# Performance work log

Hardware: AMD Instinct MI355X
Metric: run time of the kernel (lower is better)

The kernel has to match this reference:

```python
import jax, jax.numpy as jnp
import numpy as np
from jax import lax

B, C, H, W, HEADS = 2, 256, 192, 256, 8
HS = C // 2  # hidden_size per axial branch


def setup_inputs() -> dict:
    key = jax.random.key(0)
    ks = jax.random.split(key, 12)
    f = lambda k, shape, s=0.02: jax.random.normal(k, shape, jnp.float32) * s
    return {
        "x": jax.random.normal(ks[0], (B, C, H, W), jnp.float32),
        "ln1_g": jnp.ones((C,), jnp.float32),
        "ln1_b": jnp.zeros((C,), jnp.float32),
        "conv_in_w": f(ks[1], (C, C)),
        "conv_in_b": jnp.zeros((C,), jnp.float32),
        "qkv_h_w": f(ks[2], (3 * HS, HS)),
        "qkv_h_b": jnp.zeros((3 * HS,), jnp.float32),
        "qkv_v_w": f(ks[3], (3 * HS, HS)),
        "qkv_v_b": jnp.zeros((3 * HS,), jnp.float32),
        "fuse_w": f(ks[4], (C, C)),
        "fuse_b": jnp.zeros((C,), jnp.float32),
        "ln2_g": jnp.ones((C,), jnp.float32),
        "ln2_b": jnp.zeros((C,), jnp.float32),
        "fc1_w": f(ks[5], (4 * C, C)),
        "fc1_b": f(ks[6], (4 * C,), 1e-6),
        "fc2_w": f(ks[7], (C, 4 * C)),
        "fc2_b": f(ks[8], (C,), 1e-6),
        "peg_w": f(ks[9], (C, 1, 3, 3)),
        "peg_b": jnp.zeros((C,), jnp.float32),
    }


def _ln(x, g, b, eps=1e-5):
    m = x.mean(-1, keepdims=True)
    v = jnp.mean((x - m) ** 2, axis=-1, keepdims=True)
    return (x - m) / jnp.sqrt(v + eps) * g + b


def _mha(q, k, v, heads):
    # q,k,v: [Bn, N, Ch]
    Bn, N, Ch = q.shape
    d = Ch // heads
    q = q.reshape(Bn, N, heads, d).transpose(0, 2, 1, 3)
    k = k.reshape(Bn, N, heads, d).transpose(0, 2, 1, 3)
    v = v.reshape(Bn, N, heads, d).transpose(0, 2, 1, 3)
    scores = jnp.einsum('bhnd,bhmd->bhnm', q, k) / jnp.sqrt(jnp.float32(d))
    probs = jax.nn.softmax(scores, axis=-1)
    out = jnp.einsum('bhnm,bhmd->bhnd', probs, v)
    return out.transpose(0, 2, 1, 3).reshape(Bn, N, Ch)


def reference(x, ln1_g, ln1_b, conv_in_w, conv_in_b, qkv_h_w, qkv_h_b,
              qkv_v_w, qkv_v_b, fuse_w, fuse_b, ln2_g, ln2_b,
              fc1_w, fc1_b, fc2_w, fc2_b, peg_w, peg_b):
    Bx, Cx, Hx, Wx = x.shape
    hs = Cx // 2
    h0 = x
    # LayerNorm over channel dim
    t = x.reshape(Bx, Cx, Hx * Wx).transpose(0, 2, 1)  # [B, HW, C]
    t = _ln(t, ln1_g, ln1_b)
    xn = t.transpose(0, 2, 1).reshape(Bx, Cx, Hx, Wx)
    # 1x1 conv input
    ci = jnp.einsum('bchw,oc->bohw', xn, conv_in_w) + conv_in_b[None, :, None, None]
    # horizontal strips: [B*H, W, hs]; vertical strips: [B*W, H, hs]
    fh = ci[:, :hs].transpose(0, 2, 3, 1).reshape(Bx * Hx, Wx, hs)
    fv = ci[:, hs:].transpose(0, 3, 2, 1).reshape(Bx * Wx, Hx, hs)
    q_h, k_h, v_h = jnp.split(fh @ qkv_h_w.T + qkv_h_b, 3, axis=2)
    q_v, k_v, v_v = jnp.split(fv @ qkv_v_w.T + qkv_v_b, 3, axis=2)
    ah = _mha(q_h, k_h, v_h, HEADS)  # [B*H, W, hs]
    av = _mha(q_v, k_v, v_v, HEADS)  # [B*W, H, hs]
    ah = ah.reshape(Bx, Hx, Wx, hs).transpose(0, 3, 1, 2)  # [B, hs, H, W]
    av = av.reshape(Bx, Wx, Hx, hs).transpose(0, 3, 2, 1)  # [B, hs, H, W]
    cat = jnp.concatenate((ah, av), axis=1)  # [B, C, H, W]
    attn_out = jnp.einsum('bchw,oc->bohw', cat, fuse_w) + fuse_b[None, :, None, None]
    x1 = attn_out + h0
    # FFN
    t = x1.reshape(Bx, Cx, Hx * Wx).transpose(0, 2, 1)  # [B, HW, C]
    h1 = t
    t2 = _ln(t, ln2_g, ln2_b)
    t2 = jax.nn.gelu(t2 @ fc1_w.T + fc1_b, approximate=False)
    t2 = t2 @ fc2_w.T + fc2_b
    t = t2 + h1
    x2 = t.transpose(0, 2, 1).reshape(Bx, Cx, Hx, Wx)
    # PEG: depthwise 3x3 conv + residual
    peg = lax.conv_general_dilated(
        x2, peg_w, window_strides=(1, 1), padding='SAME',
        dimension_numbers=('NCHW', 'OIHW', 'NCHW'), feature_group_count=Cx)
    return peg + peg_b[None, :, None, None] + x2
```

## Files before the change

### kernel.cpp

```cpp
#include <hip/hip_runtime.h>

#define B_ 2
#define C_ 256
#define H_ 192
#define W_ 256
#define HW_ 49152
#define T_ 98304

typedef __bf16 bf16x8 __attribute__((ext_vector_type(8)));
typedef float  f32x4  __attribute__((ext_vector_type(4)));
typedef short  s16x8  __attribute__((ext_vector_type(8)));

__device__ inline unsigned short f2bf(float f) {
    unsigned u = __float_as_uint(f);
    u = u + 0x7fffu + ((u >> 16) & 1u);
    return (unsigned short)(u >> 16);
}
__device__ inline float bf2f(unsigned short u) {
    return __uint_as_float(((unsigned)u) << 16);
}
__device__ inline unsigned short bfbits(float f) {
    __bf16 h = (__bf16)f;
    return __builtin_bit_cast(unsigned short, h);
}
__device__ inline void gload_lds16(const unsigned short* g, short* l) {
    __builtin_amdgcn_global_load_lds(
        (const __attribute__((address_space(1))) unsigned int*)g,
        (__attribute__((address_space(3))) unsigned int*)l, 16, 0, 0);
}

__global__ __launch_bounds__(256) void wcvt_kernel(
    const float* __restrict__ in, unsigned short* __restrict__ out, int n)
{
    int i = (blockIdx.x * 256 + threadIdx.x) * 4;
    if (i >= n) return;
    float4 v = *(const float4*)(in + i);
    out[i + 0] = f2bf(v.x);
    out[i + 1] = f2bf(v.y);
    out[i + 2] = f2bf(v.z);
    out[i + 3] = f2bf(v.w);
}

__global__ __launch_bounds__(256) void ln1_stats_kernel(
    const float* __restrict__ x, float* __restrict__ mean, float* __restrict__ rstd)
{
    int t = blockIdx.x * 256 + threadIdx.x;
    int b = t / HW_;
    int hw = t - b * HW_;
    const float* p = x + (size_t)b * C_ * HW_ + hw;
    float s = 0.f, q = 0.f;
    for (int c = 0; c < C_; ++c) {
        float v = p[(size_t)c * HW_];
        s += v; q += v * v;
    }
    float m = s * (1.f / C_);
    float var = q * (1.f / C_) - m * m;
    mean[t] = m;
    rstd[t] = rsqrtf(var + 1e-5f);
}

__global__ __launch_bounds__(256) void xln_kernel(
    const float* __restrict__ x, const float* __restrict__ mean,
    const float* __restrict__ rstd, const float* __restrict__ g,
    const float* __restrict__ bta, unsigned short* __restrict__ xn)
{
    __shared__ float tile[32][33];
    int t0 = blockIdx.x * 32;
    int c0 = blockIdx.y * 32;
    int b = t0 / HW_, hw0 = t0 - b * HW_;
    int tid = threadIdx.x, lane = tid & 31, grp = tid >> 5;
    float mm = mean[t0 + lane], rr = rstd[t0 + lane];
    #pragma unroll
    for (int j = 0; j < 4; ++j) {
        int c = grp + j * 8;
        float v = x[((size_t)b * C_ + c0 + c) * HW_ + hw0 + lane];
        tile[c][lane] = (v - mm) * rr;
    }
    __syncthreads();
    float gg = g[c0 + lane], bb = bta[c0 + lane];
    #pragma unroll
    for (int j = 0; j < 4; ++j) {
        int tt = grp + j * 8;
        xn[(size_t)(t0 + tt) * C_ + c0 + lane] = f2bf(tile[lane][tt] * gg + bb);
    }
}

__global__ __launch_bounds__(256) void ln2norm_kernel(
    const float* __restrict__ xr, const float* __restrict__ g,
    const float* __restrict__ bta, unsigned short* __restrict__ out)
{
    int wv = threadIdx.x >> 6, lane = threadIdx.x & 63;
    int t = blockIdx.x * 4 + wv;
    const float4 v = *(const float4*)(xr + (size_t)t * C_ + lane * 4);
    float s = v.x + v.y + v.z + v.w;
    float q = v.x * v.x + v.y * v.y + v.z * v.z + v.w * v.w;
    #pragma unroll
    for (int o = 32; o > 0; o >>= 1) {
        s += __shfl_xor(s, o);
        q += __shfl_xor(q, o);
    }
    float m = s * (1.f / C_);
    float r = rsqrtf(q * (1.f / C_) - m * m + 1e-5f);
    float4 gg = *(const float4*)(g + lane * 4);
    float4 bb = *(const float4*)(bta + lane * 4);
    unsigned short o0 = f2bf((v.x - m) * r * gg.x + bb.x);
    unsigned short o1 = f2bf((v.y - m) * r * gg.y + bb.y);
    unsigned short o2 = f2bf((v.z - m) * r * gg.z + bb.z);
    unsigned short o3 = f2bf((v.w - m) * r * gg.w + bb.w);
    unsigned lo = ((unsigned)o1 << 16) | o0;
    unsigned hi = ((unsigned)o3 << 16) | o2;
    *(uint2*)(out + (size_t)t * C_ + lane * 4) = make_uint2(lo, hi);
}

enum { AB_ROW = 0, AB_CAT = 1, AB_GATHER = 2 };
enum { EB_BF16 = 0, EB_F32 = 1, EG_BF16 = 2, ER_F32 = 3 };

template<int AMODE, int EMODE>
__global__ __launch_bounds__(256) void mgemm(
    const unsigned short* __restrict__ A0, const unsigned short* __restrict__ A1,
    const unsigned short* __restrict__ Wb, const float* __restrict__ bias,
    const float* __restrict__ resid, float* __restrict__ outf,
    unsigned short* __restrict__ outb,
    int K, int lda, int ldw, int ldo, int rowoff)
{
    __shared__ __align__(16) short As[8][512];
    __shared__ __align__(16) short Bs[8][512];
    const int tid = threadIdx.x;
    const int t0 = blockIdx.x * 128;
    const int n0 = blockIdx.y * 128;
    const int lane = tid & 63, wv = tid >> 6;
    const int wr = wv >> 1, wc = wv & 1;
    const int fr = lane & 15;
    const int fk = (lane >> 4) * 8;

    const unsigned short* aptr0 = nullptr;
    const unsigned short* aptr1 = nullptr;
    if (AMODE == AB_GATHER) {
        #pragma unroll
        for (int si = 0; si < 2; ++si) {
            const int gr = rowoff + t0 + (wv * 2 + si) * 16 + fr;
            const int b = gr / HW_;
            const int rem = gr - b * HW_;
            const int w = rem / H_;
            const int h = rem - w * H_;
            const unsigned short* p =
                A0 + ((size_t)b * HW_ + (size_t)h * W_ + w) * 256 + 128 + fk;
            if (si == 0) aptr0 = p; else aptr1 = p;
        }
    } else if (AMODE == AB_ROW) {
        aptr0 = A0 + (size_t)(t0 + (wv * 2 + 0) * 16 + fr) * lda + fk;
        aptr1 = A0 + (size_t)(t0 + (wv * 2 + 1) * 16 + fr) * lda + fk;
    }
    const unsigned short* bptr0 = Wb + (size_t)(n0 + (wv * 2 + 0) * 16 + fr) * ldw + fk;
    const unsigned short* bptr1 = Wb + (size_t)(n0 + (wv * 2 + 1) * 16 + fr) * ldw + fk;

    f32x4 acc[4][4];
    #pragma unroll
    for (int m = 0; m < 4; ++m)
        #pragma unroll
        for (int n = 0; n < 4; ++n)
            acc[m][n] = (f32x4){0.f, 0.f, 0.f, 0.f};

    for (int k0 = 0; k0 < K; k0 += 32) {
        if (AMODE == AB_CAT) {
            const unsigned short* base = (k0 < 128) ? A0 : A1;
            const int kk = (k0 & 127) + fk;
            gload_lds16(base + (size_t)(t0 + (wv * 2 + 0) * 16 + fr) * 128 + kk,
                        &As[wv * 2 + 0][0]);
            gload_lds16(base + (size_t)(t0 + (wv * 2 + 1) * 16 + fr) * 128 + kk,
                        &As[wv * 2 + 1][0]);
        } else {
            gload_lds16(aptr0 + k0, &As[wv * 2 + 0][0]);
            gload_lds16(aptr1 + k0, &As[wv * 2 + 1][0]);
        }
        gload_lds16(bptr0 + k0, &Bs[wv * 2 + 0][0]);
        gload_lds16(bptr1 + k0, &Bs[wv * 2 + 1][0]);
        __syncthreads();
        bf16x8 af[4], bfr[4];
        #pragma unroll
        for (int m = 0; m < 4; ++m)
            af[m] = __builtin_bit_cast(bf16x8, *(const s16x8*)&As[wr * 4 + m][lane * 8]);
        #pragma unroll
        for (int n = 0; n < 4; ++n)
            bfr[n] = __builtin_bit_cast(bf16x8, *(const s16x8*)&Bs[wc * 4 + n][lane * 8]);
        #pragma unroll
        for (int m = 0; m < 4; ++m)
            #pragma unroll
            for (int n = 0; n < 4; ++n)
                acc[m][n] = __builtin_amdgcn_mfma_f32_16x16x32_bf16(
                    af[m], bfr[n], acc[m][n], 0, 0, 0);
        __syncthreads();
    }

    const int rowb = t0 + wr * 64 + (lane >> 4) * 4;
    const int colb = n0 + wc * 64 + (lane & 15);
    #pragma unroll
    for (int n = 0; n < 4; ++n) {
        const int col = colb + n * 16;
        const float bcol = bias[col];
        #pragma unroll
        for (int m = 0; m < 4; ++m) {
            #pragma unroll
            for (int r = 0; r < 4; ++r) {
                const int row = rowb + m * 16 + r;
                float v = acc[m][n][r] + bcol;
                if (EMODE == EG_BF16)
                    v = 0.5f * v * (1.f + erff(v * 0.70710678118654752f));
                if (EMODE == ER_F32)
                    v += resid[(size_t)row * 256 + col];
                if (EMODE == EB_F32 || EMODE == ER_F32)
                    outf[(size_t)row * ldo + col] = v;
                else
                    outb[(size_t)row * ldo + col] = f2bf(v);
            }
        }
    }
}

__global__ __launch_bounds__(256) void tadd_kernel(
    const float* __restrict__ x, float* __restrict__ x1)
{
    __shared__ float tile[32][33];
    int t0 = blockIdx.x * 32;
    int c0 = blockIdx.y * 32;
    int b = t0 / HW_, hw0 = t0 - b * HW_;
    int tid = threadIdx.x;
    int lane = tid & 31, grp = tid >> 5;
    #pragma unroll
    for (int j = 0; j < 4; ++j) {
        int c = grp + j * 8;
        tile[c][lane] = x[((size_t)b * C_ + c0 + c) * HW_ + hw0 + lane];
    }
    __syncthreads();
    #pragma unroll
    for (int j = 0; j < 4; ++j) {
        int tt = grp + j * 8;
        x1[(size_t)(t0 + tt) * C_ + c0 + lane] += tile[lane][tt];
    }
}

template<int N, int DIR>
__global__ __launch_bounds__(256) void attn_mfma_kernel(
    const unsigned short* __restrict__ qkv, unsigned short* __restrict__ outb, int strip0)
{
    constexpr int NT = N / 16;
    constexpr int CH = N / 32;
    constexpr int QTW = N / 64;
    constexpr int PST = N + 8;
    __shared__ __align__(16) short kls[NT * 256];
    __shared__ __align__(16) short vls[CH * 512];
    __shared__ __align__(16) short plds[4 * 16 * PST];
    const int head = blockIdx.x & 7;
    const int sl = blockIdx.x >> 3;
    const int s = strip0 + sl;
    const int tid = threadIdx.x;
    const unsigned short* base = qkv + (size_t)sl * N * 384;
    for (int i = tid; i < 2 * N; i += 256) {
        int r = i >> 1, hf = i & 1;
        s16x8 kv = *(const s16x8*)(base + (size_t)r * 384 + 128 + head * 16 + hf * 8);
        *(s16x8*)&kls[(r >> 4) * 256 + (hf * 16 + (r & 15)) * 8] = kv;
    }
    for (int i = tid; i < 2 * N; i += 256) {
        int r = i >> 1, hf = i & 1;
        s16x8 vv = *(const s16x8*)(base + (size_t)r * 384 + 256 + head * 16 + hf * 8);
        short* dst = &vls[(r >> 5) * 512 + ((r & 31) >> 3) * 128 + (r & 7)];
        #pragma unroll
        for (int j = 0; j < 8; ++j)
            dst[(hf * 8 + j) * 8] = vv[j];
    }
    __syncthreads();
    const int wv = tid >> 6, lane = tid & 63, g = lane >> 4, q = lane & 15;
    short* myP = &plds[wv * 16 * PST];
    const bf16x8 zf = __builtin_bit_cast(bf16x8, (s16x8){0,0,0,0,0,0,0,0});
    for (int qt_i = 0; qt_i < QTW; ++qt_i) {
        const int q0 = wv * (N / 4) + qt_i * 16;
        bf16x8 qf = zf;
        if (lane < 32)
            qf = __builtin_bit_cast(bf16x8,
                *(const s16x8*)(base + (size_t)(q0 + q) * 384 + head * 16 + g * 8));
        f32x4 sc[NT];
        #pragma unroll
        for (int n = 0; n < NT; ++n) {
            bf16x8 kf = zf;
            if (lane < 32)
                kf = __builtin_bit_cast(bf16x8, *(const s16x8*)&kls[n * 256 + lane * 8]);
            sc[n] = __builtin_amdgcn_mfma_f32_16x16x32_bf16(
                kf, qf, (f32x4){0.f, 0.f, 0.f, 0.f}, 0, 0, 0);
        }
        float mx = -3.0e38f;
        #pragma unroll
        for (int n = 0; n < NT; ++n)
            mx = fmaxf(mx, fmaxf(fmaxf(sc[n][0], sc[n][1]), fmaxf(sc[n][2], sc[n][3])));
        mx = fmaxf(mx, __shfl_xor(mx, 16));
        mx = fmaxf(mx, __shfl_xor(mx, 32));
        float sum = 0.f;
        #pragma unroll
        for (int n = 0; n < NT; ++n) {
            float p0 = __expf((sc[n][0] - mx) * 0.25f);
            float p1 = __expf((sc[n][1] - mx) * 0.25f);
            float p2 = __expf((sc[n][2] - mx) * 0.25f);
            float p3 = __expf((sc[n][3] - mx) * 0.25f);
            sum += (p0 + p1) + (p2 + p3);
            unsigned u01 = ((unsigned)bfbits(p1) << 16) | bfbits(p0);
            unsigned u23 = ((unsigned)bfbits(p3) << 16) | bfbits(p2);
            *(unsigned*)&myP[q * PST + n * 16 + g * 4] = u01;
            *(unsigned*)&myP[q * PST + n * 16 + g * 4 + 2] = u23;
        }
        sum += __shfl_xor(sum, 16);
        sum += __shfl_xor(sum, 32);
        const float inv = 1.f / sum;
        f32x4 o = (f32x4){0.f, 0.f, 0.f, 0.f};
        #pragma unroll
        for (int c = 0; c < CH; ++c) {
            bf16x8 vf = __builtin_bit_cast(bf16x8, *(const s16x8*)&vls[c * 512 + lane * 8]);
            bf16x8 pf = __builtin_bit_cast(bf16x8, *(const s16x8*)&myP[q * PST + c * 32 + g * 8]);
            o = __builtin_amdgcn_mfma_f32_16x16x32_bf16(vf, pf, o, 0, 0, 0);
        }
        unsigned lo = ((unsigned)bfbits(o[1] * inv) << 16) | bfbits(o[0] * inv);
        unsigned hi = ((unsigned)bfbits(o[3] * inv) << 16) | bfbits(o[2] * inv);
        size_t dst;
        if (DIR == 0) {
            dst = ((size_t)s * W_ + q0 + q) * 128 + head * 16 + g * 4;
        } else {
            int b = s >> 8, w = s & 255;
            dst = ((size_t)b * HW_ + (size_t)(q0 + q) * W_ + w) * 128 + head * 16 + g * 4;
        }
        *(uint2*)&outb[dst] = make_uint2(lo, hi);
    }
}

__global__ __launch_bounds__(256) void peg_kernel(
    const float* __restrict__ x2t, const float* __restrict__ pw,
    const float* __restrict__ pb, float* __restrict__ outp)
{
    __shared__ float pwt[9][132];
    __shared__ float tile[32][132];
    const int t0 = blockIdx.x * 32;
    const int cbase = blockIdx.y * 128;
    const int b = t0 / HW_, hw0 = t0 - b * HW_;
    const int h = hw0 >> 8, w0 = hw0 & 255;
    const int tid = threadIdx.x;
    for (int i = tid; i < 1152; i += 256) {
        int tap = i >> 7, ch = i & 127;
        pwt[tap][ch] = pw[(size_t)(cbase + ch) * 9 + tap];
    }
    __syncthreads();
    const int c4 = tid & 31;
    const int tg = tid >> 5;
    const int cq = cbase + c4 * 4;
    float4 pb4 = *(const float4*)(pb + cq);
    #pragma unroll
    for (int j = 0; j < 4; ++j) {
        int tt = tg * 4 + j;
        int t = t0 + tt;
        int w = w0 + tt;
        float4 a = *(const float4*)(x2t + (size_t)t * C_ + cq);
        a.x += pb4.x; a.y += pb4.y; a.z += pb4.z; a.w += pb4.w;
        #pragma unroll
        for (int dh = -1; dh <= 1; ++dh) {
            int hh = h + dh;
            if (hh < 0 || hh >= H_) continue;
            #pragma unroll
            for (int dw = -1; dw <= 1; ++dw) {
                int ww = w + dw;
                if (ww < 0 || ww >= W_) continue;
                float4 xv = *(const float4*)(x2t + (size_t)(t + dh * W_ + dw) * C_ + cq);
                float4 wvv = *(const float4*)&pwt[(dh + 1) * 3 + (dw + 1)][c4 * 4];
                a.x += wvv.x * xv.x; a.y += wvv.y * xv.y;
                a.z += wvv.z * xv.z; a.w += wvv.w * xv.w;
            }
        }
        *(float4*)&tile[tt][c4 * 4] = a;
    }
    __syncthreads();
    const int ch = tid >> 1, hf = (tid & 1) * 16;
    float* drow = outp + ((size_t)b * C_ + cbase + ch) * HW_ + hw0 + hf;
    #pragma unroll
    for (int qq = 0; qq < 4; ++qq) {
        float4 vv = make_float4(tile[hf + qq * 4 + 0][ch], tile[hf + qq * 4 + 1][ch],
                                tile[hf + qq * 4 + 2][ch], tile[hf + qq * 4 + 3][ch]);
        *(float4*)(drow + qq * 4) = vv;
    }
}

extern "C" void kernel_launch(void* const* d_in, const int* in_sizes, int n_in,
                              void* d_out, int out_size, void* d_ws, size_t ws_size,
                              hipStream_t stream)
{
    (void)in_sizes; (void)n_in; (void)out_size; (void)ws_size;
    const float* x         = (const float*)d_in[0];
    const float* ln1_g     = (const float*)d_in[1];
    const float* ln1_b     = (const float*)d_in[2];
    const float* conv_in_w = (const float*)d_in[3];
    const float* conv_in_b = (const float*)d_in[4];
    const float* qkv_h_w   = (const float*)d_in[5];
    const float* qkv_h_b   = (const float*)d_in[6];
    const float* qkv_v_w   = (const float*)d_in[7];
    const float* qkv_v_b   = (const float*)d_in[8];
    const float* fuse_w    = (const float*)d_in[9];
    const float* fuse_b    = (const float*)d_in[10];
    const float* ln2_g     = (const float*)d_in[11];
    const float* ln2_b     = (const float*)d_in[12];
    const float* fc1_w     = (const float*)d_in[13];
    const float* fc1_b     = (const float*)d_in[14];
    const float* fc2_w     = (const float*)d_in[15];
    const float* fc2_b     = (const float*)d_in[16];
    const float* peg_w     = (const float*)d_in[17];
    const float* peg_b     = (const float*)d_in[18];
    float* outp = (float*)d_out;

    float* wsf   = (float*)d_ws;
    float* mean1 = wsf;
    float* rstd1 = wsf + (size_t)T_;
    float* x1    = wsf + 2 * (size_t)T_;
    unsigned short* xn = (unsigned short*)x1;
    unsigned short* ci = (unsigned short*)(x1 + (size_t)T_ * 128);
    unsigned short* ah = (unsigned short*)(x1 + (size_t)T_ * 256);
    unsigned short* av = ah + (size_t)T_ * 128;
    unsigned short* xn2 = ah;
    unsigned short* qt = av + (size_t)T_ * 128;
    unsigned short* wb = qt + (size_t)24576 * 1024;
    unsigned short* wconv = wb;
    unsigned short* wqh   = wconv + 65536;
    unsigned short* wqv   = wqh + 49152;
    unsigned short* wfu   = wqv + 49152;
    unsigned short* wf1   = wfu + 65536;
    unsigned short* wf2   = wf1 + 262144;

    dim3 blk(256);

    wcvt_kernel<<<dim3(64), blk, 0, stream>>>(conv_in_w, wconv, 65536);
    wcvt_kernel<<<dim3(48), blk, 0, stream>>>(qkv_h_w, wqh, 49152);
    wcvt_kernel<<<dim3(48), blk, 0, stream>>>(qkv_v_w, wqv, 49152);
    wcvt_kernel<<<dim3(64), blk, 0, stream>>>(fuse_w, wfu, 65536);
    wcvt_kernel<<<dim3(256), blk, 0, stream>>>(fc1_w, wf1, 262144);
    wcvt_kernel<<<dim3(256), blk, 0, stream>>>(fc2_w, wf2, 262144);
    ln1_stats_kernel<<<dim3(T_ / 256), blk, 0, stream>>>(x, mean1, rstd1);
    xln_kernel<<<dim3(T_ / 32, 8), blk, 0, stream>>>(x, mean1, rstd1, ln1_g, ln1_b, xn);
    mgemm<AB_ROW, EB_BF16><<<dim3(768, 2), blk, 0, stream>>>(
        xn, nullptr, wconv, conv_in_b, nullptr, nullptr, ci, 256, 256, 256, 256, 0);
    for (int ch = 0; ch < 2; ++ch) {
        const size_t r0 = (size_t)ch * 49152;
        mgemm<AB_ROW, EB_BF16><<<dim3(384, 3), blk, 0, stream>>>(
            ci + r0 * 256, nullptr, wqh, qkv_h_b, nullptr, nullptr, qt,
            128, 256, 128, 384, 0);
        attn_mfma_kernel<256, 0><<<dim3(192 * 8), blk, 0, stream>>>(qt, ah, ch * 192);
    }
    for (int cv = 0; cv < 2; ++cv) {
        mgemm<AB_GATHER, EB_BF16><<<dim3(384, 3), blk, 0, stream>>>(
            ci, nullptr, wqv, qkv_v_b, nullptr, nullptr, qt,
            128, 0, 128, 384, cv * 49152);
        attn_mfma_kernel<192, 1><<<dim3(256 * 8), blk, 0, stream>>>(qt, av, cv * 256);
    }
    mgemm<AB_CAT, EB_F32><<<dim3(768, 2), blk, 0, stream>>>(
        ah, av, wfu, fuse_b, nullptr, x1, nullptr, 256, 128, 256, 256, 0);
    tadd_kernel<<<dim3(T_ / 32, 8), blk, 0, stream>>>(x, x1);
    ln2norm_kernel<<<dim3(T_ / 4), blk, 0, stream>>>(x1, ln2_g, ln2_b, xn2);
    for (int cs = 0; cs < 4; ++cs) {
        const size_t r0 = (size_t)cs * 24576;
        mgemm<AB_ROW, EG_BF16><<<dim3(192, 8), blk, 0, stream>>>(
            xn2 + r0 * 256, nullptr, wf1, fc1_b, nullptr, nullptr, qt,
            256, 256, 256, 1024, 0);
        mgemm<AB_ROW, ER_F32><<<dim3(192, 2), blk, 0, stream>>>(
            qt, nullptr, wf2, fc2_b, x1 + r0 * 256, x1 + r0 * 256, nullptr,
            1024, 1024, 1024, 256, 0);
    }
    peg_kernel<<<dim3(T_ / 32, 2), blk, 0, stream>>>(x1, peg_w, peg_b, outp);
}
```

Baseline: 1.075 ms.

## Double-buffer GEMM LDS staging and fuse planar residual add into fuse GEMM

The mgemm K-loop now uses two LDS buffers, so the global-to-LDS load of the next K slice is issued before the MFMAs on the current slice and one barrier per iteration is removed. Separately, the NCHW residual add of x is folded into the fuse-projection GEMM epilogue through a new planar-residual mode that reads float4 along HW, which removes the separate transpose-add kernel and its extra read and write of x1. Doubling LDS per block to 32KB may lower occupancy.

```diff
diff --git a/kernel.cpp b/kernel.cpp
--- a/kernel.cpp
+++ b/kernel.cpp
@@ -113,7 +113,7 @@
 }
 
 enum { AB_ROW = 0, AB_CAT = 1, AB_GATHER = 2 };
-enum { EB_BF16 = 0, EB_F32 = 1, EG_BF16 = 2, ER_F32 = 3 };
+enum { EB_BF16 = 0, EB_F32 = 1, EG_BF16 = 2, ER_F32 = 3, ER_PLANAR = 4 };
 
 template<int AMODE, int EMODE>
 __global__ __launch_bounds__(256) void mgemm(
@@ -123,8 +123,8 @@
     unsigned short* __restrict__ outb,
     int K, int lda, int ldw, int ldo, int rowoff)
 {
-    __shared__ __align__(16) short As[8][512];
-    __shared__ __align__(16) short Bs[8][512];
+    __shared__ __align__(16) short As[2][8][512];
+    __shared__ __align__(16) short Bs[2][8][512];
     const int tid = threadIdx.x;
     const int t0 = blockIdx.x * 128;
     const int n0 = blockIdx.y * 128;
@@ -161,36 +161,49 @@
         for (int n = 0; n < 4; ++n)
             acc[m][n] = (f32x4){0.f, 0.f, 0.f, 0.f};
 
-    for (int k0 = 0; k0 < K; k0 += 32) {
+    auto stage = [&](int buf, int k0) {
         if (AMODE == AB_CAT) {
             const unsigned short* base = (k0 < 128) ? A0 : A1;
             const int kk = (k0 & 127) + fk;
             gload_lds16(base + (size_t)(t0 + (wv * 2 + 0) * 16 + fr) * 128 + kk,
-                        &As[wv * 2 + 0][0]);
+                        &As[buf][wv * 2 + 0][0]);
             gload_lds16(base + (size_t)(t0 + (wv * 2 + 1) * 16 + fr) * 128 + kk,
-                        &As[wv * 2 + 1][0]);
+                        &As[buf][wv * 2 + 1][0]);
         } else {
-            gload_lds16(aptr0 + k0, &As[wv * 2 + 0][0]);
-            gload_lds16(aptr1 + k0, &As[wv * 2 + 1][0]);
-        }
-        gload_lds16(bptr0 + k0, &Bs[wv * 2 + 0][0]);
-        gload_lds16(bptr1 + k0, &Bs[wv * 2 + 1][0]);
-        __syncthreads();
+            gload_lds16(aptr0 + k0, &As[buf][wv * 2 + 0][0]);
+            gload_lds16(aptr1 + k0, &As[buf][wv * 2 + 1][0]);
+        }
+        gload_lds16(bptr0 + k0, &Bs[buf][wv * 2 + 0][0]);
+        gload_lds16(bptr1 + k0, &Bs[buf][wv * 2 + 1][0]);
+    };
+    auto compute = [&](int buf) {
         bf16x8 af[4], bfr[4];
         #pragma unroll
         for (int m = 0; m < 4; ++m)
-            af[m] = __builtin_bit_cast(bf16x8, *(const s16x8*)&As[wr * 4 + m][lane * 8]);
+            af[m] = __builtin_bit_cast(bf16x8,
+                *(const s16x8*)&As[buf][wr * 4 + m][lane * 8]);
         #pragma unroll
         for (int n = 0; n < 4; ++n)
-            bfr[n] = __builtin_bit_cast(bf16x8, *(const s16x8*)&Bs[wc * 4 + n][lane * 8]);
+            bfr[n] = __builtin_bit_cast(bf16x8,
+                *(const s16x8*)&Bs[buf][wc * 4 + n][lane * 8]);
         #pragma unroll
         for (int m = 0; m < 4; ++m)
             #pragma unroll
             for (int n = 0; n < 4; ++n)
                 acc[m][n] = __builtin_amdgcn_mfma_f32_16x16x32_bf16(
                     af[m], bfr[n], acc[m][n], 0, 0, 0);
+    };
+
+    stage(0, 0);
+    __syncthreads();
+    int cur = 0;
+    for (int k0 = 32; k0 < K; k0 += 32) {
+        stage(cur ^ 1, k0);
+        compute(cur);
         __syncthreads();
-    }
+        cur ^= 1;
+    }
+    compute(cur);
 
     const int rowb = t0 + wr * 64 + (lane >> 4) * 4;
     const int colb = n0 + wc * 64 + (lane & 15);
@@ -200,42 +213,29 @@
         const float bcol = bias[col];
         #pragma unroll
         for (int m = 0; m < 4; ++m) {
+            const int row0 = rowb + m * 16;
+            float4 rv = make_float4(0.f, 0.f, 0.f, 0.f);
+            if (EMODE == ER_PLANAR) {
+                const int bb = (row0 >= HW_) ? 1 : 0;
+                const int hw = row0 - bb * HW_;
+                rv = *(const float4*)(resid + ((size_t)bb * C_ + col) * HW_ + hw);
+            }
             #pragma unroll
             for (int r = 0; r < 4; ++r) {
-                const int row = rowb + m * 16 + r;
+                const int row = row0 + r;
                 float v = acc[m][n][r] + bcol;
                 if (EMODE == EG_BF16)
                     v = 0.5f * v * (1.f + erff(v * 0.70710678118654752f));
                 if (EMODE == ER_F32)
                     v += resid[(size_t)row * 256 + col];
-                if (EMODE == EB_F32 || EMODE == ER_F32)
+                if (EMODE == ER_PLANAR)
+                    v += (&rv.x)[r];
+                if (EMODE == EB_F32 || EMODE == ER_F32 || EMODE == ER_PLANAR)
                     outf[(size_t)row * ldo + col] = v;
                 else
                     outb[(size_t)row * ldo + col] = f2bf(v);
             }
         }
-    }
-}
-
-__global__ __launch_bounds__(256) void tadd_kernel(
-    const float* __restrict__ x, float* __restrict__ x1)
-{
-    __shared__ float tile[32][33];
-    int t0 = blockIdx.x * 32;
-    int c0 = blockIdx.y * 32;
-    int b = t0 / HW_, hw0 = t0 - b * HW_;
-    int tid = threadIdx.x;
-    int lane = tid & 31, grp = tid >> 5;
-    #pragma unroll
-    for (int j = 0; j < 4; ++j) {
-        int c = grp + j * 8;
-        tile[c][lane] = x[((size_t)b * C_ + c0 + c) * HW_ + hw0 + lane];
-    }
-    __syncthreads();
-    #pragma unroll
-    for (int j = 0; j < 4; ++j) {
-        int tt = grp + j * 8;
-        x1[(size_t)(t0 + tt) * C_ + c0 + lane] += tile[lane][tt];
     }
 }
 
@@ -452,9 +452,8 @@
             128, 0, 128, 384, cv * 49152);
         attn_mfma_kernel<192, 1><<<dim3(256 * 8), blk, 0, stream>>>(qt, av, cv * 256);
     }
-    mgemm<AB_CAT, EB_F32><<<dim3(768, 2), blk, 0, stream>>>(
-        ah, av, wfu, fuse_b, nullptr, x1, nullptr, 256, 128, 256, 256, 0);
-    tadd_kernel<<<dim3(T_ / 32, 8), blk, 0, stream>>>(x, x1);
+    mgemm<AB_CAT, ER_PLANAR><<<dim3(768, 2), blk, 0, stream>>>(
+        ah, av, wfu, fuse_b, x, x1, nullptr, 256, 128, 256, 256, 0);
     ln2norm_kernel<<<dim3(T_ / 4), blk, 0, stream>>>(x1, ln2_g, ln2_b, xn2);
     for (int cs = 0; cs < 4; ++cs) {
         const size_t r0 = (size_t)cs * 24576;
```

After: 1.090 ms. About the same (+1.4%).
